# Optimization experiments

Measured on AMD Instinct MI355X. Metric: run time of the kernel, lower is better.

The kernel has to match this reference:

```python
import jax, jax.numpy as jnp
import numpy as np

N, R, L, H, D, E = 30000, 3, 4, 128, 128, 20000  # nodes, ranks, max group len, hidden, input_dim, n_hyperedges
NUM_HEADS = 4


def _xavier(rng, fan_in, fan_out, shape=None):
    bound = np.sqrt(6.0 / (fan_in + fan_out))
    shape = (fan_in, fan_out) if shape is None else shape
    return jnp.asarray(rng.uniform(-bound, bound, size=shape), dtype=jnp.float32)


def setup_inputs() -> dict:
    rng = np.random.default_rng(0)
    # hyperedge id h has rank h % R; ids of rank r are r + R*k
    deg = 1 + (np.arange(N * R).reshape(N, R) % L)          # per (node, rank) group size in 1..L
    mask = np.arange(L)[None, None, :] < deg[:, :, None]    # [N,R,L] valid slots
    ks = rng.integers(0, E // R, size=(N, R, L))
    he_idx = ks * R + np.arange(R)[None, :, None]           # hyperedge ids matching each rank row
    he_idx = np.where(mask, he_idx, 0)
    valid_idx = np.flatnonzero(mask.reshape(-1)).astype(np.int64)  # [nnz], nnz = 225000
    # he_order: per-node argsort of its (rank-ordered) valid hyperedge id list, plus running offset
    flatm = mask.reshape(N, R * L)
    row_vals = np.where(flatm, he_idx.reshape(N, R * L), E + 1)
    perm = np.argsort(row_vals, axis=1, kind='stable')      # positions of sorted values
    compact = np.cumsum(flatm, axis=1) - 1                   # padded pos -> compact (valid-list) index
    deg_total = flatm.sum(1)
    offsets = np.concatenate([[0], np.cumsum(deg_total)[:-1]])
    compact_at_perm = np.take_along_axis(compact, perm, axis=1)
    take = np.arange(R * L)[None, :] < deg_total[:, None]
    he_order = (compact_at_perm + offsets[:, None])[take].astype(np.int64)
    inp = {
        'x_rank': jnp.asarray(rng.standard_normal((N, R, D)), jnp.float32),
        'he_features': jnp.asarray(rng.standard_normal((E, H)), jnp.float32),
        'he_idx': jnp.asarray(he_idx, jnp.int32),
        'valid_idx': jnp.asarray(valid_idx, jnp.int32),
        'he_order': jnp.asarray(he_order, jnp.int32),
        # GRU gate parameters (whh: hidden->hidden, wxh: input->hidden, b: hidden)
        'r_whh': _xavier(rng, H, H), 'r_wxh': _xavier(rng, D, H), 'r_b': jnp.zeros((H,), jnp.float32),
        'u_whh': _xavier(rng, H, H), 'u_wxh': _xavier(rng, D, H), 'u_b': jnp.zeros((H,), jnp.float32),
        'c_whh': _xavier(rng, H, H), 'c_wxh': _xavier(rng, D, H), 'c_b': jnp.zeros((H,), jnp.float32),
        # MultiheadAttention params (torch layout: in_proj_weight [3H,H])
        'in_proj_w': _xavier(rng, 3 * H, H, shape=(3 * H, H)),
        'in_proj_b': jnp.zeros((3 * H,), jnp.float32),
        'out_w': _xavier(rng, H, H, shape=(H, H)),
        'out_b': jnp.zeros((H,), jnp.float32),
    }
    return inp


def reference(x_rank, he_features, he_idx, valid_idx, he_order,
              r_whh, r_wxh, r_b, u_whh, u_wxh, u_b, c_whh, c_wxh, c_b,
              in_proj_w, in_proj_b, out_w, out_b):
    n, n_ranks, _ = x_rank.shape
    hd = H // NUM_HEADS

    # ---- GRU over ranks (sequence axis) ----
    def step(h, x_t):
        r = jax.nn.sigmoid(h @ r_whh + x_t @ r_wxh + r_b)
        z = jax.nn.sigmoid(h @ u_whh + x_t @ u_wxh + u_b)
        c = jnp.tanh((r * h) @ c_whh + x_t @ c_wxh + c_b)  # (r*h)@W per python precedence
        h = z * c + (1.0 - z) * h
        return h, h

    h0 = jnp.zeros((n, H), x_rank.dtype)
    _, hs = jax.lax.scan(step, h0, jnp.swapaxes(x_rank, 0, 1))  # [R,N,H]
    hs = jnp.swapaxes(hs, 0, 1)                                  # [N,R,H]

    # ---- ragged gather-pad + per (node, rank) MHA with a single key/value ----
    wq, wk, wv = in_proj_w[:H], in_proj_w[H:2 * H], in_proj_w[2 * H:]
    bq, bk, bv = in_proj_b[:H], in_proj_b[H:2 * H], in_proj_b[2 * H:]
    q = he_features[he_idx]                                       # [N,R,L,H]
    qp = (q @ wq.T + bq).reshape(n, n_ranks, L, NUM_HEADS, hd)
    kp = (hs @ wk.T + bk).reshape(n, n_ranks, NUM_HEADS, hd)
    vp = (hs @ wv.T + bv).reshape(n, n_ranks, NUM_HEADS, hd)
    scale = 1.0 / jnp.sqrt(jnp.asarray(hd, q.dtype))
    scores = jnp.einsum('nrlhd,nrhd->nrlh', qp, kp) * scale       # key length is 1
    attn = jax.nn.softmax(scores[..., None], axis=-1)[..., 0]     # softmax over singleton key axis -> 1
    ctx = attn[..., None] * vp[:, :, None]                        # [N,R,L,heads,hd]
    out = ctx.reshape(n, n_ranks, L, H) @ out_w.T + out_b         # [N,R,L,H]
    # select valid (non-padded) slots, concatenated in node/rank order
    result = out.reshape(-1, H)[valid_idx]                        # [nnz,H]
    return result, he_order
```

## Files before the change

### kernel.cpp

```cpp
#include <hip/hip_runtime.h>
#include <math.h>

#define Hd 128
#define Rr 3
#define Ll 4
#define NPW 16
#define NW  8

typedef float f32x4 __attribute__((ext_vector_type(4)));
typedef short s16x8 __attribute__((ext_vector_type(8)));

__device__ __forceinline__ unsigned short f2bf(float f){
    unsigned u = __float_as_uint(f);
    return (unsigned short)((u + 0x7FFFu + ((u >> 16) & 1u)) >> 16);
}
__device__ __forceinline__ s16x8 cvt8(const float* p){
    float4 a = *(const float4*)p;
    float4 b = *(const float4*)(p + 4);
    float v[8] = {a.x, a.y, a.z, a.w, b.x, b.y, b.z, b.w};
    s16x8 r;
    #pragma unroll
    for (int j = 0; j < 8; ++j) r[j] = (short)f2bf(v[j]);
    return r;
}
__device__ __forceinline__ int lower_bound_i32(const int* __restrict__ a, int n, int key){
    int lo = 0, hi = n;
    while (lo < hi){
        int mid = (lo + hi) >> 1;
        if (a[mid] < key) lo = mid + 1; else hi = mid;
    }
    return lo;
}

__device__ __forceinline__ void gload_lds16(const unsigned short* g, unsigned short* l){
    __builtin_amdgcn_global_load_lds(
        (const __attribute__((address_space(1))) void*)g,
        (__attribute__((address_space(3))) void*)l, 16, 0, 0);
}

__global__ void fold_proj_kernel(const float* __restrict__ in_proj_w,
                                 const float* __restrict__ in_proj_b,
                                 const float* __restrict__ out_w,
                                 const float* __restrict__ out_b,
                                 float* __restrict__ McT,
                                 float* __restrict__ bc)
{
    const int i = blockIdx.x;
    const int j = threadIdx.x;
    float acc = 0.f;
    for (int k = 0; k < Hd; ++k)
        acc = fmaf(out_w[j * Hd + k], in_proj_w[(2 * Hd + k) * Hd + i], acc);
    McT[i * Hd + j] = acc;
    if (i == 0){
        float b = out_b[j];
        for (int k = 0; k < Hd; ++k)
            b = fmaf(out_w[j * Hd + k], in_proj_b[2 * Hd + k], b);
        bc[j] = b;
    }
}

__global__ void pack_kernel(const float* __restrict__ r_whh, const float* __restrict__ u_whh,
                            const float* __restrict__ r_wxh, const float* __restrict__ u_wxh,
                            const float* __restrict__ c_whh, const float* __restrict__ c_wxh,
                            const float* __restrict__ McT,
                            unsigned short* __restrict__ whi)
{
    const int mat  = blockIdx.y;
    const int tile = blockIdx.x;
    const int l    = threadIdx.x;
    const float* W;
    switch (mat){
        case 0: W = r_whh; break;  case 1: W = u_whh; break;
        case 2: W = r_wxh; break;  case 3: W = u_wxh; break;
        case 4: W = c_whh; break;  case 5: W = c_wxh; break;
        default: W = McT;
    }
    const int kc = tile >> 3, nc = tile & 7;
    const int kbase = kc * 32 + (l >> 4) * 8;
    const int n = nc * 16 + (l & 15);
    const size_t obase = ((size_t)(mat * 32 + tile) * 64 + l) * 8;
    #pragma unroll
    for (int j = 0; j < 8; ++j)
        whi[obase + j] = f2bf(W[(kbase + j) * Hd + n]);
}

#define BF_LDS(kc, nc) (*(const s16x8*)&WL[cur][(((kc) * 8 + (nc)) * 64 + l) * 8])

#define MM1(acc, AH, BH)                                                  \
    acc = __builtin_amdgcn_mfma_f32_16x16x32_bf16(AH, BH, acc, 0, 0, 0);

__global__ __launch_bounds__(512, 1) void gru_mfma_kernel(
    const float* __restrict__ x_rank,
    const int* __restrict__ valid_idx, int nv,
    const float* __restrict__ r_b, const float* __restrict__ u_b, const float* __restrict__ c_b,
    const unsigned short* __restrict__ whi,
    const float* __restrict__ bc,
    float* __restrict__ out, int N)
{
    __shared__ __align__(16) unsigned short WL[2][16384];
    __shared__ __align__(16) float Sr_all[NW][NPW][132];
    __shared__ float bias_s[4][Hd];
    __shared__ int lo_all[NW][NPW];
    __shared__ int hi_all[NW][NPW];

    const int tid = threadIdx.x;
    const int wid = tid >> 6;
    const int l   = tid & 63;
    const int lr  = l & 15;
    const int lg  = l >> 4;
    const int n0  = (blockIdx.x * NW + wid) * NPW;

    float (*Sr)[132] = Sr_all[wid];
    int* loL = lo_all[wid];
    int* hiL = hi_all[wid];

    if (tid < Hd){
        bias_s[0][tid] = r_b[tid];
        bias_s[1][tid] = u_b[tid];
        bias_s[2][tid] = c_b[tid];
        bias_s[3][tid] = bc[tid];
    }

    #define STAGE_MAT(mat, b)                                                    \
        {                                                                        \
            const unsigned short* msrc = whi + (size_t)(mat) * 16384;            \
            _Pragma("unroll")                                                    \
            for (int it = 0; it < 4; ++it){                                      \
                const int chunk = it * 8 + wid;                                  \
                gload_lds16(msrc + chunk * 512 + l * 8, &WL[b][chunk * 512]);    \
            }                                                                    \
        }

    f32x4 hD[8];
    s16x8 ah[4];
    #pragma unroll
    for (int nc = 0; nc < 8; ++nc) hD[nc] = (f32x4){0.f, 0.f, 0.f, 0.f};
    #pragma unroll
    for (int kc = 0; kc < 4; ++kc) ah[kc] = (s16x8)0;

    s16x8 xh[4], rhh[4];

    unsigned cur = 0;
    STAGE_MAT(0, 0);

    #pragma unroll 1
    for (int t = 0; t < Rr; ++t){
        if (l < NPW){
            int n = n0 + l, lo = 0, hi = 0;
            if (n < N){
                int F = (n * Rr + t) * Ll;
                lo = lower_bound_i32(valid_idx, nv, F);
                hi = lower_bound_i32(valid_idx, nv, F + Ll);
            }
            loL[l] = lo; hiL[l] = hi;
        }

        {
            int nn = n0 + lr; if (nn > N - 1) nn = N - 1;
            const float* xp = x_rank + ((size_t)nn * Rr + t) * Hd;
            #pragma unroll
            for (int kc = 0; kc < 4; ++kc)
                xh[kc] = cvt8(xp + kc * 32 + lg * 8);
        }

        f32x4 accR[8], accZ[8];

        __syncthreads();
        STAGE_MAT(2, cur ^ 1);
        #pragma unroll
        for (int nc = 0; nc < 8; ++nc){
            accR[nc] = (f32x4){0.f, 0.f, 0.f, 0.f};
            #pragma unroll
            for (int kc = 0; kc < 4; ++kc){ s16x8 b = BF_LDS(kc, nc); MM1(accR[nc], ah[kc], b); }
            if ((nc & 3) == 3) __builtin_amdgcn_sched_barrier(0);
        }
        cur ^= 1;

        __syncthreads();
        STAGE_MAT(1, cur ^ 1);
        #pragma unroll
        for (int nc = 0; nc < 8; ++nc){
            #pragma unroll
            for (int kc = 0; kc < 4; ++kc){ s16x8 b = BF_LDS(kc, nc); MM1(accR[nc], xh[kc], b); }
            const float rbc = bias_s[0][nc * 16 + lr];
            #pragma unroll
            for (int i = 0; i < 4; ++i){
                float r = 1.f / (1.f + __expf(-(accR[nc][i] + rbc)));
                Sr[lg * 4 + i][nc * 16 + lr] = r * hD[nc][i];
            }
            if ((nc & 3) == 3) __builtin_amdgcn_sched_barrier(0);
        }
        cur ^= 1;

        __syncthreads();
        STAGE_MAT(3, cur ^ 1);
        #pragma unroll
        for (int nc = 0; nc < 8; ++nc){
            accZ[nc] = (f32x4){0.f, 0.f, 0.f, 0.f};
            #pragma unroll
            for (int kc = 0; kc < 4; ++kc){ s16x8 b = BF_LDS(kc, nc); MM1(accZ[nc], ah[kc], b); }
            if ((nc & 3) == 3) __builtin_amdgcn_sched_barrier(0);
        }
        cur ^= 1;

        __syncthreads();
        STAGE_MAT(4, cur ^ 1);
        #pragma unroll
        for (int nc = 0; nc < 8; ++nc){
            #pragma unroll
            for (int kc = 0; kc < 4; ++kc){ s16x8 b = BF_LDS(kc, nc); MM1(accZ[nc], xh[kc], b); }
            const float ubc = bias_s[1][nc * 16 + lr];
            #pragma unroll
            for (int i = 0; i < 4; ++i)
                accZ[nc][i] = 1.f / (1.f + __expf(-(accZ[nc][i] + ubc)));
            if ((nc & 3) == 3) __builtin_amdgcn_sched_barrier(0);
        }
        cur ^= 1;

        __syncthreads();
        STAGE_MAT(5, cur ^ 1);
        #pragma unroll
        for (int kc = 0; kc < 4; ++kc)
            rhh[kc] = cvt8(&Sr[lr][kc * 32 + lg * 8]);
        f32x4 accC[8];
        #pragma unroll
        for (int nc = 0; nc < 8; ++nc){
            accC[nc] = (f32x4){0.f, 0.f, 0.f, 0.f};
            #pragma unroll
            for (int kc = 0; kc < 4; ++kc){ s16x8 b = BF_LDS(kc, nc); MM1(accC[nc], rhh[kc], b); }
            if ((nc & 3) == 3) __builtin_amdgcn_sched_barrier(0);
        }
        cur ^= 1;

        __syncthreads();
        STAGE_MAT(6, cur ^ 1);
        #pragma unroll
        for (int nc = 0; nc < 8; ++nc){
            #pragma unroll
            for (int kc = 0; kc < 4; ++kc){ s16x8 b = BF_LDS(kc, nc); MM1(accC[nc], xh[kc], b); }
            const float cbc = bias_s[2][nc * 16 + lr];
            #pragma unroll
            for (int i = 0; i < 4; ++i){
                float e = __expf(2.f * (accC[nc][i] + cbc));
                float c = 1.f - 2.f / (e + 1.f);
                float ho = hD[nc][i];
                float hn = ho + accZ[nc][i] * (c - ho);
                hD[nc][i] = hn;
                Sr[lg * 4 + i][nc * 16 + lr] = hn;
            }
            if ((nc & 3) == 3) __builtin_amdgcn_sched_barrier(0);
        }
        #pragma unroll
        for (int kc = 0; kc < 4; ++kc)
            ah[kc] = cvt8(&Sr[lr][kc * 32 + lg * 8]);
        cur ^= 1;

        __syncthreads();
        if (t < Rr - 1) STAGE_MAT(0, cur ^ 1);
        #pragma unroll
        for (int nc = 0; nc < 8; ++nc){
            f32x4 ao = (f32x4){0.f, 0.f, 0.f, 0.f};
            #pragma unroll
            for (int kc = 0; kc < 4; ++kc){ s16x8 b = BF_LDS(kc, nc); MM1(ao, ah[kc], b); }
            const float obc = bias_s[3][nc * 16 + lr];
            #pragma unroll
            for (int i = 0; i < 4; ++i)
                Sr[lg * 4 + i][nc * 16 + lr] = ao[i] + obc;
            if ((nc & 3) == 3) __builtin_amdgcn_sched_barrier(0);
        }
        __builtin_amdgcn_sched_barrier(0);

        #pragma unroll
        for (int m = 0; m < 8; ++m){
            const int row = m * 2 + (l >> 5);
            const int c4  = (l & 31) * 4;
            const float4 v = *(const float4*)&Sr[row][c4];
            const int lo = loL[row], hi = hiL[row];
            for (int rr = lo; rr < hi; ++rr)
                *(float4*)(out + (size_t)rr * Hd + c4) = v;
        }
        cur ^= 1;
    }
    #undef STAGE_MAT
}

__global__ void he_order_kernel(const int* __restrict__ he_order,
                                float* __restrict__ out_tail, int nv)
{
    const int i = blockIdx.x * 256 + threadIdx.x;
    if (i < nv) out_tail[i] = (float)he_order[i];
}

extern "C" void kernel_launch(void* const* d_in, const int* in_sizes, int n_in,
                              void* d_out, int out_size, void* d_ws, size_t ws_size,
                              hipStream_t stream)
{
    const float* x_rank    = (const float*)d_in[0];
    const int*   valid_idx = (const int*)d_in[3];
    const int*   he_order  = (const int*)d_in[4];
    const float* r_whh = (const float*)d_in[5];
    const float* r_wxh = (const float*)d_in[6];
    const float* r_b   = (const float*)d_in[7];
    const float* u_whh = (const float*)d_in[8];
    const float* u_wxh = (const float*)d_in[9];
    const float* u_b   = (const float*)d_in[10];
    const float* c_whh = (const float*)d_in[11];
    const float* c_wxh = (const float*)d_in[12];
    const float* c_b   = (const float*)d_in[13];
    const float* in_proj_w = (const float*)d_in[14];
    const float* in_proj_b = (const float*)d_in[15];
    const float* out_w     = (const float*)d_in[16];
    const float* out_b     = (const float*)d_in[17];

    const int nv = in_sizes[3];
    const int N  = in_sizes[0] / (Rr * Hd);

    float* McT = (float*)d_ws;
    float* bc  = McT + Hd * Hd;
    unsigned short* whi = (unsigned short*)(bc + Hd);

    float* out_f    = (float*)d_out;
    float* out_tail = out_f + (size_t)nv * Hd;

    fold_proj_kernel<<<Hd, Hd, 0, stream>>>(in_proj_w, in_proj_b, out_w, out_b, McT, bc);
    pack_kernel<<<dim3(32, 7), 64, 0, stream>>>(r_whh, u_whh, r_wxh, u_wxh, c_whh, c_wxh,
                                                McT, whi);

    const int nodes_per_block = NW * NPW;
    const int nblocks = (N + nodes_per_block - 1) / nodes_per_block;
    gru_mfma_kernel<<<nblocks, 512, 0, stream>>>(
        x_rank, valid_idx, nv, r_b, u_b, c_b, whi, bc, out_f, N);

    he_order_kernel<<<(nv + 255) / 256, 256, 0, stream>>>(he_order, out_tail, nv);
}
```

Baseline: 97.28 us.

## Process two 16-row M tiles per wave to reuse LDS weight fragments

Each wave now handles 32 nodes as two 16-row MFMA tiles, with 4 waves per block instead of 8. Every weight fragment read from LDS feeds two MFMAs, which halves LDS read traffic per MFMA. The update gate z is now kept in the shared Sr buffer rather than in registers, to offset the doubled accumulator and hidden-state register footprint. The trade-off is fewer waves per CU for hiding latency, plus extra LDS stores and loads for z.

```diff
diff --git a/kernel.cpp b/kernel.cpp
--- a/kernel.cpp
+++ b/kernel.cpp
@@ -4,8 +4,8 @@
 #define Hd 128
 #define Rr 3
 #define Ll 4
-#define NPW 16
-#define NW  8
+#define NPW 32
+#define NW  4
 
 typedef float f32x4 __attribute__((ext_vector_type(4)));
 typedef short s16x8 __attribute__((ext_vector_type(8)));
@@ -89,7 +89,7 @@
 #define MM1(acc, AH, BH)                                                  \
     acc = __builtin_amdgcn_mfma_f32_16x16x32_bf16(AH, BH, acc, 0, 0, 0);
 
-__global__ __launch_bounds__(512, 1) void gru_mfma_kernel(
+__global__ __launch_bounds__(256, 1) void gru_mfma_kernel(
     const float* __restrict__ x_rank,
     const int* __restrict__ valid_idx, int nv,
     const float* __restrict__ r_b, const float* __restrict__ u_b, const float* __restrict__ c_b,
@@ -125,20 +125,22 @@
         {                                                                        \
             const unsigned short* msrc = whi + (size_t)(mat) * 16384;            \
             _Pragma("unroll")                                                    \
-            for (int it = 0; it < 4; ++it){                                      \
-                const int chunk = it * 8 + wid;                                  \
+            for (int it = 0; it < 8; ++it){                                      \
+                const int chunk = it * 4 + wid;                                  \
                 gload_lds16(msrc + chunk * 512 + l * 8, &WL[b][chunk * 512]);    \
             }                                                                    \
         }
 
-    f32x4 hD[8];
-    s16x8 ah[4];
+    f32x4 hD[2][8];
+    s16x8 ah[2][4];
     #pragma unroll
-    for (int nc = 0; nc < 8; ++nc) hD[nc] = (f32x4){0.f, 0.f, 0.f, 0.f};
-    #pragma unroll
-    for (int kc = 0; kc < 4; ++kc) ah[kc] = (s16x8)0;
-
-    s16x8 xh[4], rhh[4];
+    for (int mt = 0; mt < 2; ++mt){
+        #pragma unroll
+        for (int nc = 0; nc < 8; ++nc) hD[mt][nc] = (f32x4){0.f, 0.f, 0.f, 0.f};
+        #pragma unroll
+        for (int kc = 0; kc < 4; ++kc) ah[mt][kc] = (s16x8)0;
+    }
+    s16x8 xh[2][4], rhh[2][4];
 
     unsigned cur = 0;
     STAGE_MAT(0, 0);
@@ -155,23 +157,28 @@
             loL[l] = lo; hiL[l] = hi;
         }
 
-        {
-            int nn = n0 + lr; if (nn > N - 1) nn = N - 1;
+        #pragma unroll
+        for (int mt = 0; mt < 2; ++mt){
+            int nn = n0 + mt * 16 + lr; if (nn > N - 1) nn = N - 1;
             const float* xp = x_rank + ((size_t)nn * Rr + t) * Hd;
             #pragma unroll
             for (int kc = 0; kc < 4; ++kc)
-                xh[kc] = cvt8(xp + kc * 32 + lg * 8);
-        }
-
-        f32x4 accR[8], accZ[8];
+                xh[mt][kc] = cvt8(xp + kc * 32 + lg * 8);
+        }
 
         __syncthreads();
         STAGE_MAT(2, cur ^ 1);
-        #pragma unroll
-        for (int nc = 0; nc < 8; ++nc){
-            accR[nc] = (f32x4){0.f, 0.f, 0.f, 0.f};
-            #pragma unroll
-            for (int kc = 0; kc < 4; ++kc){ s16x8 b = BF_LDS(kc, nc); MM1(accR[nc], ah[kc], b); }
+        f32x4 accR[2][8];
+        #pragma unroll
+        for (int nc = 0; nc < 8; ++nc){
+            accR[0][nc] = (f32x4){0.f, 0.f, 0.f, 0.f};
+            accR[1][nc] = (f32x4){0.f, 0.f, 0.f, 0.f};
+            #pragma unroll
+            for (int kc = 0; kc < 4; ++kc){
+                s16x8 b = BF_LDS(kc, nc);
+                MM1(accR[0][nc], ah[0][kc], b);
+                MM1(accR[1][nc], ah[1][kc], b);
+            }
             if ((nc & 3) == 3) __builtin_amdgcn_sched_barrier(0);
         }
         cur ^= 1;
@@ -181,97 +188,142 @@
         #pragma unroll
         for (int nc = 0; nc < 8; ++nc){
             #pragma unroll
-            for (int kc = 0; kc < 4; ++kc){ s16x8 b = BF_LDS(kc, nc); MM1(accR[nc], xh[kc], b); }
+            for (int kc = 0; kc < 4; ++kc){
+                s16x8 b = BF_LDS(kc, nc);
+                MM1(accR[0][nc], xh[0][kc], b);
+                MM1(accR[1][nc], xh[1][kc], b);
+            }
             const float rbc = bias_s[0][nc * 16 + lr];
             #pragma unroll
+            for (int mt = 0; mt < 2; ++mt)
+                #pragma unroll
+                for (int i = 0; i < 4; ++i){
+                    float r = 1.f / (1.f + __expf(-(accR[mt][nc][i] + rbc)));
+                    Sr[mt * 16 + lg * 4 + i][nc * 16 + lr] = r * hD[mt][nc][i];
+                }
+            if ((nc & 3) == 3) __builtin_amdgcn_sched_barrier(0);
+        }
+        cur ^= 1;
+
+        __syncthreads();
+        STAGE_MAT(3, cur ^ 1);
+        f32x4 accZ[2][8];
+        #pragma unroll
+        for (int nc = 0; nc < 8; ++nc){
+            accZ[0][nc] = (f32x4){0.f, 0.f, 0.f, 0.f};
+            accZ[1][nc] = (f32x4){0.f, 0.f, 0.f, 0.f};
+            #pragma unroll
+            for (int kc = 0; kc < 4; ++kc){
+                s16x8 b = BF_LDS(kc, nc);
+                MM1(accZ[0][nc], ah[0][kc], b);
+                MM1(accZ[1][nc], ah[1][kc], b);
+            }
+            if ((nc & 3) == 3) __builtin_amdgcn_sched_barrier(0);
+        }
+        cur ^= 1;
+
+        __syncthreads();
+        STAGE_MAT(4, cur ^ 1);
+        #pragma unroll
+        for (int mt = 0; mt < 2; ++mt)
+            #pragma unroll
+            for (int kc = 0; kc < 4; ++kc)
+                rhh[mt][kc] = cvt8(&Sr[mt * 16 + lr][kc * 32 + lg * 8]);
+        __builtin_amdgcn_sched_barrier(0);
+        #pragma unroll
+        for (int nc = 0; nc < 8; ++nc){
+            #pragma unroll
+            for (int kc = 0; kc < 4; ++kc){
+                s16x8 b = BF_LDS(kc, nc);
+                MM1(accZ[0][nc], xh[0][kc], b);
+                MM1(accZ[1][nc], xh[1][kc], b);
+            }
+            const float ubc = bias_s[1][nc * 16 + lr];
+            #pragma unroll
+            for (int mt = 0; mt < 2; ++mt)
+                #pragma unroll
+                for (int i = 0; i < 4; ++i){
+                    float z = 1.f / (1.f + __expf(-(accZ[mt][nc][i] + ubc)));
+                    Sr[mt * 16 + lg * 4 + i][nc * 16 + lr] = z;
+                }
+            if ((nc & 3) == 3) __builtin_amdgcn_sched_barrier(0);
+        }
+        cur ^= 1;
+
+        __syncthreads();
+        STAGE_MAT(5, cur ^ 1);
+        f32x4 accC[2][8];
+        #pragma unroll
+        for (int nc = 0; nc < 8; ++nc){
+            accC[0][nc] = (f32x4){0.f, 0.f, 0.f, 0.f};
+            accC[1][nc] = (f32x4){0.f, 0.f, 0.f, 0.f};
+            #pragma unroll
+            for (int kc = 0; kc < 4; ++kc){
+                s16x8 b = BF_LDS(kc, nc);
+                MM1(accC[0][nc], rhh[0][kc], b);
+                MM1(accC[1][nc], rhh[1][kc], b);
+            }
+            if ((nc & 3) == 3) __builtin_amdgcn_sched_barrier(0);
+        }
+        cur ^= 1;
+
+        __syncthreads();
+        STAGE_MAT(6, cur ^ 1);
+        #pragma unroll
+        for (int nc = 0; nc < 8; ++nc){
+            #pragma unroll
+            for (int kc = 0; kc < 4; ++kc){
+                s16x8 b = BF_LDS(kc, nc);
+                MM1(accC[0][nc], xh[0][kc], b);
+                MM1(accC[1][nc], xh[1][kc], b);
+            }
+            const float cbc = bias_s[2][nc * 16 + lr];
+            #pragma unroll
+            for (int mt = 0; mt < 2; ++mt)
+                #pragma unroll
+                for (int i = 0; i < 4; ++i){
+                    const int row = mt * 16 + lg * 4 + i, col = nc * 16 + lr;
+                    float e = __expf(2.f * (accC[mt][nc][i] + cbc));
+                    float c = 1.f - 2.f / (e + 1.f);
+                    float z  = Sr[row][col];
+                    float ho = hD[mt][nc][i];
+                    float hn = ho + z * (c - ho);
+                    hD[mt][nc][i] = hn;
+                    Sr[row][col] = hn;
+                }
+            if ((nc & 3) == 3) __builtin_amdgcn_sched_barrier(0);
+        }
+        #pragma unroll
+        for (int mt = 0; mt < 2; ++mt)
+            #pragma unroll
+            for (int kc = 0; kc < 4; ++kc)
+                ah[mt][kc] = cvt8(&Sr[mt * 16 + lr][kc * 32 + lg * 8]);
+        cur ^= 1;
+
+        __syncthreads();
+        if (t < Rr - 1) STAGE_MAT(0, cur ^ 1);
+        #pragma unroll
+        for (int nc = 0; nc < 8; ++nc){
+            f32x4 ao0 = (f32x4){0.f, 0.f, 0.f, 0.f};
+            f32x4 ao1 = (f32x4){0.f, 0.f, 0.f, 0.f};
+            #pragma unroll
+            for (int kc = 0; kc < 4; ++kc){
+                s16x8 b = BF_LDS(kc, nc);
+                MM1(ao0, ah[0][kc], b);
+                MM1(ao1, ah[1][kc], b);
+            }
+            const float obc = bias_s[3][nc * 16 + lr];
+            #pragma unroll
             for (int i = 0; i < 4; ++i){
-                float r = 1.f / (1.f + __expf(-(accR[nc][i] + rbc)));
-                Sr[lg * 4 + i][nc * 16 + lr] = r * hD[nc][i];
-            }
-            if ((nc & 3) == 3) __builtin_amdgcn_sched_barrier(0);
-        }
-        cur ^= 1;
-
-        __syncthreads();
-        STAGE_MAT(3, cur ^ 1);
-        #pragma unroll
-        for (int nc = 0; nc < 8; ++nc){
-            accZ[nc] = (f32x4){0.f, 0.f, 0.f, 0.f};
-            #pragma unroll
-            for (int kc = 0; kc < 4; ++kc){ s16x8 b = BF_LDS(kc, nc); MM1(accZ[nc], ah[kc], b); }
-            if ((nc & 3) == 3) __builtin_amdgcn_sched_barrier(0);
-        }
-        cur ^= 1;
-
-        __syncthreads();
-        STAGE_MAT(4, cur ^ 1);
-        #pragma unroll
-        for (int nc = 0; nc < 8; ++nc){
-            #pragma unroll
-            for (int kc = 0; kc < 4; ++kc){ s16x8 b = BF_LDS(kc, nc); MM1(accZ[nc], xh[kc], b); }
-            const float ubc = bias_s[1][nc * 16 + lr];
-            #pragma unroll
-            for (int i = 0; i < 4; ++i)
-                accZ[nc][i] = 1.f / (1.f + __expf(-(accZ[nc][i] + ubc)));
-            if ((nc & 3) == 3) __builtin_amdgcn_sched_barrier(0);
-        }
-        cur ^= 1;
-
-        __syncthreads();
-        STAGE_MAT(5, cur ^ 1);
-        #pragma unroll
-        for (int kc = 0; kc < 4; ++kc)
-            rhh[kc] = cvt8(&Sr[lr][kc * 32 + lg * 8]);
-        f32x4 accC[8];
-        #pragma unroll
-        for (int nc = 0; nc < 8; ++nc){
-            accC[nc] = (f32x4){0.f, 0.f, 0.f, 0.f};
-            #pragma unroll
-            for (int kc = 0; kc < 4; ++kc){ s16x8 b = BF_LDS(kc, nc); MM1(accC[nc], rhh[kc], b); }
-            if ((nc & 3) == 3) __builtin_amdgcn_sched_barrier(0);
-        }
-        cur ^= 1;
-
-        __syncthreads();
-        STAGE_MAT(6, cur ^ 1);
-        #pragma unroll
-        for (int nc = 0; nc < 8; ++nc){
-            #pragma unroll
-            for (int kc = 0; kc < 4; ++kc){ s16x8 b = BF_LDS(kc, nc); MM1(accC[nc], xh[kc], b); }
-            const float cbc = bias_s[2][nc * 16 + lr];
-            #pragma unroll
-            for (int i = 0; i < 4; ++i){
-                float e = __expf(2.f * (accC[nc][i] + cbc));
-                float c = 1.f - 2.f / (e + 1.f);
-                float ho = hD[nc][i];
-                float hn = ho + accZ[nc][i] * (c - ho);
-                hD[nc][i] = hn;
-                Sr[lg * 4 + i][nc * 16 + lr] = hn;
-            }
-            if ((nc & 3) == 3) __builtin_amdgcn_sched_barrier(0);
-        }
-        #pragma unroll
-        for (int kc = 0; kc < 4; ++kc)
-            ah[kc] = cvt8(&Sr[lr][kc * 32 + lg * 8]);
-        cur ^= 1;
-
-        __syncthreads();
-        if (t < Rr - 1) STAGE_MAT(0, cur ^ 1);
-        #pragma unroll
-        for (int nc = 0; nc < 8; ++nc){
-            f32x4 ao = (f32x4){0.f, 0.f, 0.f, 0.f};
-            #pragma unroll
-            for (int kc = 0; kc < 4; ++kc){ s16x8 b = BF_LDS(kc, nc); MM1(ao, ah[kc], b); }
-            const float obc = bias_s[3][nc * 16 + lr];
-            #pragma unroll
-            for (int i = 0; i < 4; ++i)
-                Sr[lg * 4 + i][nc * 16 + lr] = ao[i] + obc;
+                Sr[lg * 4 + i][nc * 16 + lr]      = ao0[i] + obc;
+                Sr[16 + lg * 4 + i][nc * 16 + lr] = ao1[i] + obc;
+            }
             if ((nc & 3) == 3) __builtin_amdgcn_sched_barrier(0);
         }
         __builtin_amdgcn_sched_barrier(0);
 
         #pragma unroll
-        for (int m = 0; m < 8; ++m){
+        for (int m = 0; m < 16; ++m){
             const int row = m * 2 + (l >> 5);
             const int c4  = (l & 31) * 4;
             const float4 v = *(const float4*)&Sr[row][c4];
@@ -328,7 +380,7 @@
 
     const int nodes_per_block = NW * NPW;
     const int nblocks = (N + nodes_per_block - 1) / nodes_per_block;
-    gru_mfma_kernel<<<nblocks, 512, 0, stream>>>(
+    gru_mfma_kernel<<<nblocks, 256, 0, stream>>>(
         x_rank, valid_idx, nv, r_b, u_b, c_b, whi, bc, out_f, N);
 
     he_order_kernel<<<(nv + 255) / 256, 256, 0, stream>>>(he_order, out_tail, nv);
```

Result: slower. 111.2 us (+14.3%).

## Shrink LDS footprint: single weight buffer, bf16 scratch, 4-wave blocks

Applied to the files above, without the earlier changes.

Replaces the double-buffered LDS weight staging with a single buffer, so each matrix load now waits on a barrier instead of overlapping with the MFMAs. The per-wave scratch tile is stored in bf16 instead of fp32, and blocks shrink from 8 to 4 waves. Together these cut LDS per block substantially, which is meant to let more blocks reside per CU. The cost is extra barriers and exposed global-to-LDS latency on every stage. The final projection output now also passes through bf16 before being written, which lowers output precision.

```diff
diff --git a/kernel.cpp b/kernel.cpp
--- a/kernel.cpp
+++ b/kernel.cpp
@@ -5,7 +5,8 @@
 #define Rr 3
 #define Ll 4
 #define NPW 16
-#define NW  8
+#define NW  4
+#define SRP 136
 
 typedef float f32x4 __attribute__((ext_vector_type(4)));
 typedef short s16x8 __attribute__((ext_vector_type(8)));
@@ -13,6 +14,9 @@
 __device__ __forceinline__ unsigned short f2bf(float f){
     unsigned u = __float_as_uint(f);
     return (unsigned short)((u + 0x7FFFu + ((u >> 16) & 1u)) >> 16);
+}
+__device__ __forceinline__ float bf2f(unsigned short h){
+    return __uint_as_float(((unsigned)h) << 16);
 }
 __device__ __forceinline__ s16x8 cvt8(const float* p){
     float4 a = *(const float4*)p;
@@ -84,12 +88,12 @@
         whi[obase + j] = f2bf(W[(kbase + j) * Hd + n]);
 }
 
-#define BF_LDS(kc, nc) (*(const s16x8*)&WL[cur][(((kc) * 8 + (nc)) * 64 + l) * 8])
+#define BF_LDS(kc, nc) (*(const s16x8*)&WL[(((kc) * 8 + (nc)) * 64 + l) * 8])
 
 #define MM1(acc, AH, BH)                                                  \
     acc = __builtin_amdgcn_mfma_f32_16x16x32_bf16(AH, BH, acc, 0, 0, 0);
 
-__global__ __launch_bounds__(512, 1) void gru_mfma_kernel(
+__global__ __launch_bounds__(256, 1) void gru_mfma_kernel(
     const float* __restrict__ x_rank,
     const int* __restrict__ valid_idx, int nv,
     const float* __restrict__ r_b, const float* __restrict__ u_b, const float* __restrict__ c_b,
@@ -97,8 +101,8 @@
     const float* __restrict__ bc,
     float* __restrict__ out, int N)
 {
-    __shared__ __align__(16) unsigned short WL[2][16384];
-    __shared__ __align__(16) float Sr_all[NW][NPW][132];
+    __shared__ __align__(16) unsigned short WL[16384];
+    __shared__ __align__(16) unsigned short Sr_all[NW][NPW][SRP];
     __shared__ float bias_s[4][Hd];
     __shared__ int lo_all[NW][NPW];
     __shared__ int hi_all[NW][NPW];
@@ -110,7 +114,7 @@
     const int lg  = l >> 4;
     const int n0  = (blockIdx.x * NW + wid) * NPW;
 
-    float (*Sr)[132] = Sr_all[wid];
+    unsigned short (*Sr)[SRP] = Sr_all[wid];
     int* loL = lo_all[wid];
     int* hiL = hi_all[wid];
 
@@ -121,13 +125,13 @@
         bias_s[3][tid] = bc[tid];
     }
 
-    #define STAGE_MAT(mat, b)                                                    \
+    #define STAGE_MAT(mat)                                                       \
         {                                                                        \
             const unsigned short* msrc = whi + (size_t)(mat) * 16384;            \
             _Pragma("unroll")                                                    \
-            for (int it = 0; it < 4; ++it){                                      \
-                const int chunk = it * 8 + wid;                                  \
-                gload_lds16(msrc + chunk * 512 + l * 8, &WL[b][chunk * 512]);    \
+            for (int it = 0; it < 8; ++it){                                      \
+                const int chunk = it * 4 + wid;                                  \
+                gload_lds16(msrc + chunk * 512 + l * 8, &WL[chunk * 512]);       \
             }                                                                    \
         }
 
@@ -137,11 +141,9 @@
     for (int nc = 0; nc < 8; ++nc) hD[nc] = (f32x4){0.f, 0.f, 0.f, 0.f};
     #pragma unroll
     for (int kc = 0; kc < 4; ++kc) ah[kc] = (s16x8)0;
-
     s16x8 xh[4], rhh[4];
 
-    unsigned cur = 0;
-    STAGE_MAT(0, 0);
+    STAGE_MAT(0);
 
     #pragma unroll 1
     for (int t = 0; t < Rr; ++t){
@@ -154,7 +156,6 @@
             }
             loL[l] = lo; hiL[l] = hi;
         }
-
         {
             int nn = n0 + lr; if (nn > N - 1) nn = N - 1;
             const float* xp = x_rank + ((size_t)nn * Rr + t) * Hd;
@@ -166,7 +167,6 @@
         f32x4 accR[8], accZ[8];
 
         __syncthreads();
-        STAGE_MAT(2, cur ^ 1);
         #pragma unroll
         for (int nc = 0; nc < 8; ++nc){
             accR[nc] = (f32x4){0.f, 0.f, 0.f, 0.f};
@@ -174,10 +174,10 @@
             for (int kc = 0; kc < 4; ++kc){ s16x8 b = BF_LDS(kc, nc); MM1(accR[nc], ah[kc], b); }
             if ((nc & 3) == 3) __builtin_amdgcn_sched_barrier(0);
         }
-        cur ^= 1;
-
-        __syncthreads();
-        STAGE_MAT(1, cur ^ 1);
+        __syncthreads();
+        STAGE_MAT(2);
+
+        __syncthreads();
         #pragma unroll
         for (int nc = 0; nc < 8; ++nc){
             #pragma unroll
@@ -186,14 +186,14 @@
             #pragma unroll
             for (int i = 0; i < 4; ++i){
                 float r = 1.f / (1.f + __expf(-(accR[nc][i] + rbc)));
-                Sr[lg * 4 + i][nc * 16 + lr] = r * hD[nc][i];
+                Sr[lg * 4 + i][nc * 16 + lr] = f2bf(r * hD[nc][i]);
             }
             if ((nc & 3) == 3) __builtin_amdgcn_sched_barrier(0);
         }
-        cur ^= 1;
-
-        __syncthreads();
-        STAGE_MAT(3, cur ^ 1);
+        __syncthreads();
+        STAGE_MAT(1);
+
+        __syncthreads();
         #pragma unroll
         for (int nc = 0; nc < 8; ++nc){
             accZ[nc] = (f32x4){0.f, 0.f, 0.f, 0.f};
@@ -201,10 +201,10 @@
             for (int kc = 0; kc < 4; ++kc){ s16x8 b = BF_LDS(kc, nc); MM1(accZ[nc], ah[kc], b); }
             if ((nc & 3) == 3) __builtin_amdgcn_sched_barrier(0);
         }
-        cur ^= 1;
-
-        __syncthreads();
-        STAGE_MAT(4, cur ^ 1);
+        __syncthreads();
+        STAGE_MAT(3);
+
+        __syncthreads();
         #pragma unroll
         for (int nc = 0; nc < 8; ++nc){
             #pragma unroll
@@ -215,13 +215,13 @@
                 accZ[nc][i] = 1.f / (1.f + __expf(-(accZ[nc][i] + ubc)));
             if ((nc & 3) == 3) __builtin_amdgcn_sched_barrier(0);
         }
-        cur ^= 1;
-
-        __syncthreads();
-        STAGE_MAT(5, cur ^ 1);
+        __syncthreads();
+        STAGE_MAT(4);
+
+        __syncthreads();
         #pragma unroll
         for (int kc = 0; kc < 4; ++kc)
-            rhh[kc] = cvt8(&Sr[lr][kc * 32 + lg * 8]);
+            rhh[kc] = *(const s16x8*)&Sr[lr][kc * 32 + lg * 8];
         f32x4 accC[8];
         #pragma unroll
         for (int nc = 0; nc < 8; ++nc){
@@ -230,10 +230,10 @@
             for (int kc = 0; kc < 4; ++kc){ s16x8 b = BF_LDS(kc, nc); MM1(accC[nc], rhh[kc], b); }
             if ((nc & 3) == 3) __builtin_amdgcn_sched_barrier(0);
         }
-        cur ^= 1;
-
-        __syncthreads();
-        STAGE_MAT(6, cur ^ 1);
+        __syncthreads();
+        STAGE_MAT(5);
+
+        __syncthreads();
         #pragma unroll
         for (int nc = 0; nc < 8; ++nc){
             #pragma unroll
@@ -246,17 +246,17 @@
                 float ho = hD[nc][i];
                 float hn = ho + accZ[nc][i] * (c - ho);
                 hD[nc][i] = hn;
-                Sr[lg * 4 + i][nc * 16 + lr] = hn;
+                Sr[lg * 4 + i][nc * 16 + lr] = f2bf(hn);
             }
             if ((nc & 3) == 3) __builtin_amdgcn_sched_barrier(0);
         }
         #pragma unroll
         for (int kc = 0; kc < 4; ++kc)
-            ah[kc] = cvt8(&Sr[lr][kc * 32 + lg * 8]);
-        cur ^= 1;
-
-        __syncthreads();
-        if (t < Rr - 1) STAGE_MAT(0, cur ^ 1);
+            ah[kc] = *(const s16x8*)&Sr[lr][kc * 32 + lg * 8];
+        __syncthreads();
+        STAGE_MAT(6);
+
+        __syncthreads();
         #pragma unroll
         for (int nc = 0; nc < 8; ++nc){
             f32x4 ao = (f32x4){0.f, 0.f, 0.f, 0.f};
@@ -265,21 +265,25 @@
             const float obc = bias_s[3][nc * 16 + lr];
             #pragma unroll
             for (int i = 0; i < 4; ++i)
-                Sr[lg * 4 + i][nc * 16 + lr] = ao[i] + obc;
-            if ((nc & 3) == 3) __builtin_amdgcn_sched_barrier(0);
-        }
-        __builtin_amdgcn_sched_barrier(0);
+                Sr[lg * 4 + i][nc * 16 + lr] = f2bf(ao[i] + obc);
+            if ((nc & 3) == 3) __builtin_amdgcn_sched_barrier(0);
+        }
+        __syncthreads();
+        if (t < Rr - 1) STAGE_MAT(0);
 
         #pragma unroll
         for (int m = 0; m < 8; ++m){
             const int row = m * 2 + (l >> 5);
             const int c4  = (l & 31) * 4;
-            const float4 v = *(const float4*)&Sr[row][c4];
+            const uint2 u = *(const uint2*)&Sr[row][c4];
+            float4 v = { bf2f((unsigned short)(u.x & 0xffff)),
+                         bf2f((unsigned short)(u.x >> 16)),
+                         bf2f((unsigned short)(u.y & 0xffff)),
+                         bf2f((unsigned short)(u.y >> 16)) };
             const int lo = loL[row], hi = hiL[row];
             for (int rr = lo; rr < hi; ++rr)
                 *(float4*)(out + (size_t)rr * Hd + c4) = v;
         }
-        cur ^= 1;
     }
     #undef STAGE_MAT
 }
@@ -328,7 +332,7 @@
 
     const int nodes_per_block = NW * NPW;
     const int nblocks = (N + nodes_per_block - 1) / nodes_per_block;
-    gru_mfma_kernel<<<nblocks, 512, 0, stream>>>(
+    gru_mfma_kernel<<<nblocks, 256, 0, stream>>>(
         x_rank, valid_idx, nv, r_b, u_b, c_b, whi, bc, out_f, N);
 
     he_order_kernel<<<(nv + 255) / 256, 256, 0, stream>>>(he_order, out_tail, nv);
```

Result: slower. 154.4 us (+58.8%).

## Precompute input-gate projections in a separate kernel and skip zero-state work at t=0

Applied to the files above, without the earlier changes.

Moves the x-dependent GRU gate GEMMs (r/u/c wxh plus bias) into a separate fully parallel gx_kernel that writes bf16 pre-activations to workspace. The recurrent kernel then only does the hidden-state GEMMs and reads these precomputed values. At t=0 it skips the recurrent matmuls entirely because the hidden state is zero. This trades MFMA work and weight staging inside the sequential loop for an extra kernel launch, a global round-trip of the gx buffer, and bf16 rounding of the pre-activations. A fallback path runs if the workspace is too small.

```diff
diff --git a/kernel.cpp b/kernel.cpp
--- a/kernel.cpp
+++ b/kernel.cpp
@@ -14,6 +14,9 @@
     unsigned u = __float_as_uint(f);
     return (unsigned short)((u + 0x7FFFu + ((u >> 16) & 1u)) >> 16);
 }
+__device__ __forceinline__ float bf2f(unsigned short h){
+    return __uint_as_float(((unsigned)h) << 16);
+}
 __device__ __forceinline__ s16x8 cvt8(const float* p){
     float4 a = *(const float4*)p;
     float4 b = *(const float4*)(p + 4);
@@ -31,11 +34,14 @@
     }
     return lo;
 }
-
 __device__ __forceinline__ void gload_lds16(const unsigned short* g, unsigned short* l){
     __builtin_amdgcn_global_load_lds(
         (const __attribute__((address_space(1))) void*)g,
         (__attribute__((address_space(3))) void*)l, 16, 0, 0);
+}
+__device__ __forceinline__ float gxel(uint2 u, int i){
+    unsigned w = (i < 2) ? u.x : u.y;
+    return bf2f((unsigned short)((i & 1) ? (w >> 16) : (w & 0xffff)));
 }
 
 __global__ void fold_proj_kernel(const float* __restrict__ in_proj_w,
@@ -84,42 +90,94 @@
         whi[obase + j] = f2bf(W[(kbase + j) * Hd + n]);
 }
 
-#define BF_LDS(kc, nc) (*(const s16x8*)&WL[cur][(((kc) * 8 + (nc)) * 64 + l) * 8])
-
 #define MM1(acc, AH, BH)                                                  \
     acc = __builtin_amdgcn_mfma_f32_16x16x32_bf16(AH, BH, acc, 0, 0, 0);
 
-__global__ __launch_bounds__(512, 1) void gru_mfma_kernel(
+__global__ __launch_bounds__(512, 1) void gx_kernel(
     const float* __restrict__ x_rank,
-    const int* __restrict__ valid_idx, int nv,
     const float* __restrict__ r_b, const float* __restrict__ u_b, const float* __restrict__ c_b,
     const unsigned short* __restrict__ whi,
-    const float* __restrict__ bc,
-    float* __restrict__ out, int N)
-{
-    __shared__ __align__(16) unsigned short WL[2][16384];
-    __shared__ __align__(16) float Sr_all[NW][NPW][132];
-    __shared__ float bias_s[4][Hd];
-    __shared__ int lo_all[NW][NPW];
-    __shared__ int hi_all[NW][NPW];
-
+    uint2* __restrict__ gx, int N, int NT)
+{
+    __shared__ __align__(16) unsigned short WX[3][16384];
     const int tid = threadIdx.x;
     const int wid = tid >> 6;
     const int l   = tid & 63;
     const int lr  = l & 15;
     const int lg  = l >> 4;
-    const int n0  = (blockIdx.x * NW + wid) * NPW;
+
+    const int mats[3] = {2, 3, 5};
+    #pragma unroll
+    for (int m = 0; m < 3; ++m){
+        const unsigned short* msrc = whi + (size_t)mats[m] * 16384;
+        #pragma unroll
+        for (int it = 0; it < 4; ++it){
+            const int chunk = it * 8 + wid;
+            gload_lds16(msrc + chunk * 512 + l * 8, &WX[m][chunk * 512]);
+        }
+    }
+    __syncthreads();
+
+    const int u = blockIdx.x * NW + wid;
+    if (u >= 3 * NT) return;
+    const int t  = u / NT;
+    const int nt = u % NT;
+
+    int nn = nt * NPW + lr; if (nn > N - 1) nn = N - 1;
+    const float* xp = x_rank + ((size_t)nn * Rr + t) * Hd;
+    s16x8 xh[4];
+    #pragma unroll
+    for (int kc = 0; kc < 4; ++kc)
+        xh[kc] = cvt8(xp + kc * 32 + lg * 8);
+
+    #pragma unroll
+    for (int g = 0; g < 3; ++g){
+        const float* bp = (g == 0) ? r_b : (g == 1) ? u_b : c_b;
+        #pragma unroll
+        for (int nc = 0; nc < 8; ++nc){
+            f32x4 acc = (f32x4){0.f, 0.f, 0.f, 0.f};
+            #pragma unroll
+            for (int kc = 0; kc < 4; ++kc){
+                s16x8 b = *(const s16x8*)&WX[g][(((kc) * 8 + nc) * 64 + l) * 8];
+                MM1(acc, xh[kc], b);
+            }
+            const float bb = bp[nc * 16 + lr];
+            uint2 o;
+            o.x = ((unsigned)f2bf(acc[1] + bb) << 16) | f2bf(acc[0] + bb);
+            o.y = ((unsigned)f2bf(acc[3] + bb) << 16) | f2bf(acc[2] + bb);
+            gx[(((size_t)(g * Rr + t) * NT + nt) * 8 + nc) * 64 + l] = o;
+            if ((nc & 3) == 3) __builtin_amdgcn_sched_barrier(0);
+        }
+    }
+}
+
+#define BF_LDS(kc, nc) (*(const s16x8*)&WL[cur][(((kc) * 8 + (nc)) * 64 + l) * 8])
+#define GXLD(g, t, nc) gx[(((size_t)((g) * Rr + (t)) * NT + gtile) * 8 + (nc)) * 64 + l]
+
+__global__ __launch_bounds__(512, 1) void gru_rec9_kernel(
+    const int* __restrict__ valid_idx, int nv,
+    const unsigned short* __restrict__ whi,
+    const uint2* __restrict__ gx,
+    const float* __restrict__ bc,
+    float* __restrict__ out, int N, int NT)
+{
+    __shared__ __align__(16) unsigned short WL[2][16384];
+    __shared__ __align__(16) float Sr_all[NW][NPW][132];
+    __shared__ int lo_all[NW][NPW];
+    __shared__ int hi_all[NW][NPW];
+
+    const int tid = threadIdx.x;
+    const int wid = tid >> 6;
+    const int l   = tid & 63;
+    const int lr  = l & 15;
+    const int lg  = l >> 4;
+    const int wtile = blockIdx.x * NW + wid;
+    const int n0  = wtile * NPW;
+    const int gtile = (wtile < NT) ? wtile : NT - 1;
 
     float (*Sr)[132] = Sr_all[wid];
     int* loL = lo_all[wid];
     int* hiL = hi_all[wid];
-
-    if (tid < Hd){
-        bias_s[0][tid] = r_b[tid];
-        bias_s[1][tid] = u_b[tid];
-        bias_s[2][tid] = c_b[tid];
-        bias_s[3][tid] = bc[tid];
-    }
 
     #define STAGE_MAT(mat, b)                                                    \
         {                                                                        \
@@ -132,16 +190,14 @@
         }
 
     f32x4 hD[8];
-    s16x8 ah[4];
-    #pragma unroll
-    for (int nc = 0; nc < 8; ++nc) hD[nc] = (f32x4){0.f, 0.f, 0.f, 0.f};
-    #pragma unroll
-    for (int kc = 0; kc < 4; ++kc) ah[kc] = (s16x8)0;
-
-    s16x8 xh[4], rhh[4];
+    s16x8 ah[4], rhh[4];
+    f32x4 zD[8];
+    float obc[8];
+    #pragma unroll
+    for (int nc = 0; nc < 8; ++nc) obc[nc] = bc[nc * 16 + lr];
 
     unsigned cur = 0;
-    STAGE_MAT(0, 0);
+    STAGE_MAT(6, 0);
 
     #pragma unroll 1
     for (int t = 0; t < Rr; ++t){
@@ -155,6 +211,180 @@
             loL[l] = lo; hiL[l] = hi;
         }
 
+        if (t == 0){
+            uint2 gu[8], gc[8];
+            #pragma unroll
+            for (int nc = 0; nc < 8; ++nc){ gu[nc] = GXLD(1, 0, nc); gc[nc] = GXLD(2, 0, nc); }
+            #pragma unroll
+            for (int nc = 0; nc < 8; ++nc){
+                #pragma unroll
+                for (int i = 0; i < 4; ++i){
+                    float z = 1.f / (1.f + __expf(-gxel(gu[nc], i)));
+                    float e = __expf(2.f * gxel(gc[nc], i));
+                    float c = 1.f - 2.f / (e + 1.f);
+                    float hn = z * c;
+                    hD[nc][i] = hn;
+                    Sr[lg * 4 + i][nc * 16 + lr] = hn;
+                }
+            }
+            #pragma unroll
+            for (int kc = 0; kc < 4; ++kc)
+                ah[kc] = cvt8(&Sr[lr][kc * 32 + lg * 8]);
+        } else {
+            __syncthreads();
+            STAGE_MAT(1, cur ^ 1);
+            uint2 gr[8];
+            #pragma unroll
+            for (int nc = 0; nc < 8; ++nc) gr[nc] = GXLD(0, t, nc);
+            #pragma unroll
+            for (int nc = 0; nc < 8; ++nc){
+                f32x4 accR = (f32x4){0.f, 0.f, 0.f, 0.f};
+                #pragma unroll
+                for (int kc = 0; kc < 4; ++kc){ s16x8 b = BF_LDS(kc, nc); MM1(accR, ah[kc], b); }
+                #pragma unroll
+                for (int i = 0; i < 4; ++i){
+                    float r = 1.f / (1.f + __expf(-(accR[i] + gxel(gr[nc], i))));
+                    Sr[lg * 4 + i][nc * 16 + lr] = r * hD[nc][i];
+                }
+                if ((nc & 3) == 3) __builtin_amdgcn_sched_barrier(0);
+            }
+            cur ^= 1;
+
+            __syncthreads();
+            STAGE_MAT(4, cur ^ 1);
+            uint2 gu[8];
+            #pragma unroll
+            for (int nc = 0; nc < 8; ++nc) gu[nc] = GXLD(1, t, nc);
+            #pragma unroll
+            for (int nc = 0; nc < 8; ++nc){
+                f32x4 accZ = (f32x4){0.f, 0.f, 0.f, 0.f};
+                #pragma unroll
+                for (int kc = 0; kc < 4; ++kc){ s16x8 b = BF_LDS(kc, nc); MM1(accZ, ah[kc], b); }
+                #pragma unroll
+                for (int i = 0; i < 4; ++i)
+                    zD[nc][i] = 1.f / (1.f + __expf(-(accZ[i] + gxel(gu[nc], i))));
+                if ((nc & 3) == 3) __builtin_amdgcn_sched_barrier(0);
+            }
+            #pragma unroll
+            for (int kc = 0; kc < 4; ++kc)
+                rhh[kc] = cvt8(&Sr[lr][kc * 32 + lg * 8]);
+            cur ^= 1;
+
+            __syncthreads();
+            STAGE_MAT(6, cur ^ 1);
+            uint2 gc[8];
+            #pragma unroll
+            for (int nc = 0; nc < 8; ++nc) gc[nc] = GXLD(2, t, nc);
+            #pragma unroll
+            for (int nc = 0; nc < 8; ++nc){
+                f32x4 accC = (f32x4){0.f, 0.f, 0.f, 0.f};
+                #pragma unroll
+                for (int kc = 0; kc < 4; ++kc){ s16x8 b = BF_LDS(kc, nc); MM1(accC, rhh[kc], b); }
+                #pragma unroll
+                for (int i = 0; i < 4; ++i){
+                    float e = __expf(2.f * (accC[i] + gxel(gc[nc], i)));
+                    float c = 1.f - 2.f / (e + 1.f);
+                    float ho = hD[nc][i];
+                    float hn = ho + zD[nc][i] * (c - ho);
+                    hD[nc][i] = hn;
+                    Sr[lg * 4 + i][nc * 16 + lr] = hn;
+                }
+                if ((nc & 3) == 3) __builtin_amdgcn_sched_barrier(0);
+            }
+            #pragma unroll
+            for (int kc = 0; kc < 4; ++kc)
+                ah[kc] = cvt8(&Sr[lr][kc * 32 + lg * 8]);
+            cur ^= 1;
+        }
+
+        __syncthreads();
+        if (t < Rr - 1) STAGE_MAT(0, cur ^ 1);
+        #pragma unroll
+        for (int nc = 0; nc < 8; ++nc){
+            f32x4 ao = (f32x4){0.f, 0.f, 0.f, 0.f};
+            #pragma unroll
+            for (int kc = 0; kc < 4; ++kc){ s16x8 b = BF_LDS(kc, nc); MM1(ao, ah[kc], b); }
+            #pragma unroll
+            for (int i = 0; i < 4; ++i)
+                Sr[lg * 4 + i][nc * 16 + lr] = ao[i] + obc[nc];
+            if ((nc & 3) == 3) __builtin_amdgcn_sched_barrier(0);
+        }
+        #pragma unroll
+        for (int m = 0; m < 8; ++m){
+            const int row = m * 2 + (l >> 5);
+            const int c4  = (l & 31) * 4;
+            const float4 v = *(const float4*)&Sr[row][c4];
+            const int lo = loL[row], hi = hiL[row];
+            for (int rr = lo; rr < hi; ++rr)
+                *(float4*)(out + (size_t)rr * Hd + c4) = v;
+        }
+        cur ^= 1;
+    }
+    #undef STAGE_MAT
+}
+
+__global__ __launch_bounds__(512, 1) void gru_mfma_fb(
+    const float* __restrict__ x_rank,
+    const int* __restrict__ valid_idx, int nv,
+    const float* __restrict__ r_b, const float* __restrict__ u_b, const float* __restrict__ c_b,
+    const unsigned short* __restrict__ whi,
+    const float* __restrict__ bc,
+    float* __restrict__ out, int N)
+{
+    __shared__ __align__(16) unsigned short WL[2][16384];
+    __shared__ __align__(16) float Sr_all[NW][NPW][132];
+    __shared__ float bias_s[4][Hd];
+    __shared__ int lo_all[NW][NPW];
+    __shared__ int hi_all[NW][NPW];
+
+    const int tid = threadIdx.x;
+    const int wid = tid >> 6;
+    const int l   = tid & 63;
+    const int lr  = l & 15;
+    const int lg  = l >> 4;
+    const int n0  = (blockIdx.x * NW + wid) * NPW;
+
+    float (*Sr)[132] = Sr_all[wid];
+    int* loL = lo_all[wid];
+    int* hiL = hi_all[wid];
+
+    if (tid < Hd){
+        bias_s[0][tid] = r_b[tid];
+        bias_s[1][tid] = u_b[tid];
+        bias_s[2][tid] = c_b[tid];
+        bias_s[3][tid] = bc[tid];
+    }
+    #define STAGE_MAT(mat, b)                                                    \
+        {                                                                        \
+            const unsigned short* msrc = whi + (size_t)(mat) * 16384;            \
+            _Pragma("unroll")                                                    \
+            for (int it = 0; it < 4; ++it){                                      \
+                const int chunk = it * 8 + wid;                                  \
+                gload_lds16(msrc + chunk * 512 + l * 8, &WL[b][chunk * 512]);    \
+            }                                                                    \
+        }
+    f32x4 hD[8];
+    s16x8 ah[4];
+    #pragma unroll
+    for (int nc = 0; nc < 8; ++nc) hD[nc] = (f32x4){0.f, 0.f, 0.f, 0.f};
+    #pragma unroll
+    for (int kc = 0; kc < 4; ++kc) ah[kc] = (s16x8)0;
+    s16x8 xh[4], rhh[4];
+
+    unsigned cur = 0;
+    STAGE_MAT(0, 0);
+
+    #pragma unroll 1
+    for (int t = 0; t < Rr; ++t){
+        if (l < NPW){
+            int n = n0 + l, lo = 0, hi = 0;
+            if (n < N){
+                int F = (n * Rr + t) * Ll;
+                lo = lower_bound_i32(valid_idx, nv, F);
+                hi = lower_bound_i32(valid_idx, nv, F + Ll);
+            }
+            loL[l] = lo; hiL[l] = hi;
+        }
         {
             int nn = n0 + lr; if (nn > N - 1) nn = N - 1;
             const float* xp = x_rank + ((size_t)nn * Rr + t) * Hd;
@@ -162,9 +392,7 @@
             for (int kc = 0; kc < 4; ++kc)
                 xh[kc] = cvt8(xp + kc * 32 + lg * 8);
         }
-
         f32x4 accR[8], accZ[8];
-
         __syncthreads();
         STAGE_MAT(2, cur ^ 1);
         #pragma unroll
@@ -175,7 +403,6 @@
             if ((nc & 3) == 3) __builtin_amdgcn_sched_barrier(0);
         }
         cur ^= 1;
-
         __syncthreads();
         STAGE_MAT(1, cur ^ 1);
         #pragma unroll
@@ -191,7 +418,6 @@
             if ((nc & 3) == 3) __builtin_amdgcn_sched_barrier(0);
         }
         cur ^= 1;
-
         __syncthreads();
         STAGE_MAT(3, cur ^ 1);
         #pragma unroll
@@ -202,7 +428,6 @@
             if ((nc & 3) == 3) __builtin_amdgcn_sched_barrier(0);
         }
         cur ^= 1;
-
         __syncthreads();
         STAGE_MAT(4, cur ^ 1);
         #pragma unroll
@@ -216,7 +441,6 @@
             if ((nc & 3) == 3) __builtin_amdgcn_sched_barrier(0);
         }
         cur ^= 1;
-
         __syncthreads();
         STAGE_MAT(5, cur ^ 1);
         #pragma unroll
@@ -231,7 +455,6 @@
             if ((nc & 3) == 3) __builtin_amdgcn_sched_barrier(0);
         }
         cur ^= 1;
-
         __syncthreads();
         STAGE_MAT(6, cur ^ 1);
         #pragma unroll
@@ -254,7 +477,6 @@
         for (int kc = 0; kc < 4; ++kc)
             ah[kc] = cvt8(&Sr[lr][kc * 32 + lg * 8]);
         cur ^= 1;
-
         __syncthreads();
         if (t < Rr - 1) STAGE_MAT(0, cur ^ 1);
         #pragma unroll
@@ -268,8 +490,6 @@
                 Sr[lg * 4 + i][nc * 16 + lr] = ao[i] + obc;
             if ((nc & 3) == 3) __builtin_amdgcn_sched_barrier(0);
         }
-        __builtin_amdgcn_sched_barrier(0);
-
         #pragma unroll
         for (int m = 0; m < 8; ++m){
             const int row = m * 2 + (l >> 5);
@@ -314,10 +534,14 @@
 
     const int nv = in_sizes[3];
     const int N  = in_sizes[0] / (Rr * Hd);
+    const int NT = (N + NPW - 1) / NPW;
 
     float* McT = (float*)d_ws;
     float* bc  = McT + Hd * Hd;
     unsigned short* whi = (unsigned short*)(bc + Hd);
+    const size_t base = 16384*4 + 128*4 + 7*16384*2;
+    uint2* gx = (uint2*)((char*)d_ws + base);
+    const size_t gx_bytes = (size_t)9 * NT * 8 * 64 * 8;
 
     float* out_f    = (float*)d_out;
     float* out_tail = out_f + (size_t)nv * Hd;
@@ -328,8 +552,15 @@
 
     const int nodes_per_block = NW * NPW;
     const int nblocks = (N + nodes_per_block - 1) / nodes_per_block;
-    gru_mfma_kernel<<<nblocks, 512, 0, stream>>>(
-        x_rank, valid_idx, nv, r_b, u_b, c_b, whi, bc, out_f, N);
+
+    if (ws_size >= base + gx_bytes){
+        const int gxblocks = (3 * NT + NW - 1) / NW;
+        gx_kernel<<<gxblocks, 512, 0, stream>>>(x_rank, r_b, u_b, c_b, whi, gx, N, NT);
+        gru_rec9_kernel<<<nblocks, 512, 0, stream>>>(valid_idx, nv, whi, gx, bc, out_f, N, NT);
+    } else {
+        gru_mfma_fb<<<nblocks, 512, 0, stream>>>(
+            x_rank, valid_idx, nv, r_b, u_b, c_b, whi, bc, out_f, N);
+    }
 
     he_order_kernel<<<(nv + 255) / 256, 256, 0, stream>>>(he_order, out_tail, nv);
 }
```

Result: slower. 105.4 us (+8.3%).
